# Optimization experiments

Hardware: AMD Instinct MI355X
Metric: run time of the kernel (lower is better)

The kernel has to match this reference:

```python
import jax, jax.numpy as jnp
import numpy as np

N = 50000      # num nodes
E = 800000     # num edges (before self-loops)
DIN = 256
DOUT = 256
K = 3


def setup_inputs() -> dict:
    key = jax.random.key(0)
    k1, k2, k3 = jax.random.split(key, 3)
    x = jax.random.normal(k1, (N, DIN), dtype=jnp.float32)
    edge_index = jax.random.randint(k2, (2, E), 0, N, dtype=jnp.int32)
    # xavier_uniform for weight [K+1, DIN, DOUT]
    limit = float(np.sqrt(6.0 / (DIN + DOUT)))
    weight = jax.random.uniform(k3, (K + 1, DIN, DOUT), dtype=jnp.float32,
                                minval=-limit, maxval=limit)
    bias = jnp.zeros((DOUT,), dtype=jnp.float32)
    return {"x": x, "edge_index": edge_index, "weight": weight, "bias": bias}


def reference(x, edge_index, weight, bias):
    num_nodes = x.shape[0]
    # add self loops
    loops = jnp.arange(num_nodes, dtype=edge_index.dtype)
    row = jnp.concatenate([edge_index[0], loops])
    col = jnp.concatenate([edge_index[1], loops])
    # degree of row (including self loops)
    deg = jax.ops.segment_sum(jnp.ones_like(row, dtype=x.dtype), row,
                              num_segments=num_nodes)
    deg_inv_sqrt = jnp.where(deg > 0, jax.lax.rsqrt(jnp.maximum(deg, 1e-30)), 0.0)
    # edge-weighted Laplacian values: -D^{-1/2} A D^{-1/2}, +1 on diagonal
    Lvals = -deg_inv_sqrt[row] * deg_inv_sqrt[col]
    Lvals = jnp.where(row == col, Lvals + 1.0, Lvals)

    def spmm(v):  # [N, D] -> [N, D]
        return jax.ops.segment_sum(Lvals[:, None] * v[col], row,
                                   num_segments=num_nodes)

    out = jnp.matmul(x, weight[0])
    Tx_0 = x
    Tx_1 = spmm(x)
    out = out + jnp.matmul(Tx_1, weight[1])
    for k in range(2, K + 1):
        Tx_2 = 2.0 * spmm(Tx_1) - Tx_0
        out = out + jnp.matmul(Tx_2, weight[k])
        Tx_0, Tx_1 = Tx_1, Tx_2
    return out + bias
```

## Files before the change

### kernel.cpp

```cpp
#include <hip/hip_runtime.h>
#include <hip/hip_bf16.h>

#define DFEAT 256
#define RSTRIDE 64

typedef __attribute__((ext_vector_type(8))) short bf16x8;
typedef __attribute__((ext_vector_type(4))) float f32x4;

__device__ __forceinline__ float bf2f(unsigned short u) {
  return __builtin_bit_cast(float, ((unsigned)u) << 16);
}
__device__ __forceinline__ unsigned short f2bf(float f) {
  __hip_bfloat16 h = __float2bfloat16(f);
  return *reinterpret_cast<unsigned short*>(&h);
}


__global__ void k_build(const int* __restrict__ ei0, const int* __restrict__ ei1, int E,
                        int* __restrict__ cnt, int* __restrict__ colsP) {
  int i = blockIdx.x * blockDim.x + threadIdx.x;
  if (i >= E) return;
  int r = ei0[i];
  int pos = atomicAdd(&cnt[r], 1);
  if (pos < RSTRIDE) colsP[(size_t)r * RSTRIDE + pos] = ei1[i];
}


__global__ __launch_bounds__(256) void k_f2bfwt(const float* __restrict__ x,
                                                unsigned short* __restrict__ xbf, int n4,
                                                const float* __restrict__ W,
                                                unsigned short* __restrict__ WT,
                                                const int* __restrict__ cnt,
                                                float* __restrict__ dis, int N, int nb) {
  int b = blockIdx.x;
  if (b < 256) {
    int idx = b * 256 + threadIdx.x;
    int n = idx & 255;
    int k = idx >> 8;
    float w0 = W[idx];
    float w1 = W[65536 + idx];
    float w2 = W[2 * 65536 + idx];
    float w3 = W[3 * 65536 + idx];
    int t = (n << 8) | k;
    WT[t]             = f2bf(w0 - w2);
    WT[65536 + t]     = f2bf(w1 - 3.0f * w3);
    WT[2 * 65536 + t] = f2bf(2.0f * w2);
    WT[3 * 65536 + t] = f2bf(4.0f * w3);
    return;
  }
  if (b < 256 + nb) {
    int i = (b - 256) * 256 + threadIdx.x;
    if (i < N) dis[i] = rsqrtf((float)(cnt[i] + 1));
    return;
  }
  int i = (b - 256 - nb) * 256 + threadIdx.x;
  if (i >= n4) return;
  float4 f = *(const float4*)(x + (size_t)i * 4);
  ushort4 u;
  u.x = f2bf(f.x); u.y = f2bf(f.y); u.z = f2bf(f.z); u.w = f2bf(f.w);
  *(ushort4*)(xbf + (size_t)i * 4) = u;
}


__global__ __launch_bounds__(256) void k_spmm_bf(
    const unsigned short* __restrict__ v, unsigned short* __restrict__ y,
    const int* __restrict__ cnt, const int* __restrict__ colsP,
    const float* __restrict__ dis, int N) {
  int r = blockIdx.x * 4 + (threadIdx.x >> 6);
  if (r >= N) return;
  int lane = threadIdx.x & 63;
  int fo = lane * 4;
  int len = cnt[r];
  if (len > RSTRIDE) len = RSTRIDE;
  const int* cp = colsP + (size_t)r * RSTRIDE;
  float dr = dis[r];
  float a0 = 0.f, a1 = 0.f, a2 = 0.f, a3 = 0.f;

  int e = 0;
  for (; e + 3 < len; e += 4) {
    int c0 = cp[e], c1 = cp[e + 1], c2 = cp[e + 2], c3 = cp[e + 3];
    float l0 = -dr * dis[c0] + (c0 == r ? 1.f : 0.f);
    float l1 = -dr * dis[c1] + (c1 == r ? 1.f : 0.f);
    float l2 = -dr * dis[c2] + (c2 == r ? 1.f : 0.f);
    float l3 = -dr * dis[c3] + (c3 == r ? 1.f : 0.f);
    uint2 u0 = *(const uint2*)(v + (size_t)c0 * DFEAT + fo);
    uint2 u1 = *(const uint2*)(v + (size_t)c1 * DFEAT + fo);
    uint2 u2 = *(const uint2*)(v + (size_t)c2 * DFEAT + fo);
    uint2 u3 = *(const uint2*)(v + (size_t)c3 * DFEAT + fo);
    a0 += l0 * bf2f(u0.x & 0xffff) + l1 * bf2f(u1.x & 0xffff) +
          l2 * bf2f(u2.x & 0xffff) + l3 * bf2f(u3.x & 0xffff);
    a1 += l0 * bf2f(u0.x >> 16) + l1 * bf2f(u1.x >> 16) +
          l2 * bf2f(u2.x >> 16) + l3 * bf2f(u3.x >> 16);
    a2 += l0 * bf2f(u0.y & 0xffff) + l1 * bf2f(u1.y & 0xffff) +
          l2 * bf2f(u2.y & 0xffff) + l3 * bf2f(u3.y & 0xffff);
    a3 += l0 * bf2f(u0.y >> 16) + l1 * bf2f(u1.y >> 16) +
          l2 * bf2f(u2.y >> 16) + l3 * bf2f(u3.y >> 16);
  }
  for (; e < len; ++e) {
    int c = cp[e];
    float lv = -dr * dis[c] + (c == r ? 1.f : 0.f);
    uint2 u = *(const uint2*)(v + (size_t)c * DFEAT + fo);
    a0 += lv * bf2f(u.x & 0xffff);
    a1 += lv * bf2f(u.x >> 16);
    a2 += lv * bf2f(u.y & 0xffff);
    a3 += lv * bf2f(u.y >> 16);
  }

  float sc = 1.0f - dr * dr;
  uint2 uv = *(const uint2*)(v + (size_t)r * DFEAT + fo);
  a0 += sc * bf2f(uv.x & 0xffff);
  a1 += sc * bf2f(uv.x >> 16);
  a2 += sc * bf2f(uv.y & 0xffff);
  a3 += sc * bf2f(uv.y >> 16);

  uint2 o;
  o.x = (unsigned)f2bf(a0) | ((unsigned)f2bf(a1) << 16);
  o.y = (unsigned)f2bf(a2) | ((unsigned)f2bf(a3) << 16);
  *(uint2*)(y + (size_t)r * DFEAT + fo) = o;
}


__global__ __launch_bounds__(256) void k_gemm4(
    const unsigned short* __restrict__ A0, const unsigned short* __restrict__ A1,
    const unsigned short* __restrict__ A2, const unsigned short* __restrict__ A3,
    const unsigned short* __restrict__ WT,
    const float* __restrict__ bias, float* __restrict__ C, int N) {
  int tid = threadIdx.x;
  int lane = tid & 63;
  int w = tid >> 6;
  int brow = blockIdx.x * 64;
  int arow = lane & 15;
  int kslot = (lane >> 4) * 8;

  f32x4 acc[4][4] = {};

  const unsigned short* bptr[4];
#pragma unroll
  for (int j = 0; j < 4; ++j)
    bptr[j] = WT + (size_t)(w * 64 + j * 16 + arow) * DFEAT + kslot;

#pragma unroll
  for (int g = 0; g < 4; ++g) {
    const unsigned short* Asrc = g == 0 ? A0 : g == 1 ? A1 : g == 2 ? A2 : A3;
    const unsigned short* aptr[4];
#pragma unroll
    for (int i = 0; i < 4; ++i) {
      int r = brow + i * 16 + arow;
      if (r >= N) r = N - 1;
      aptr[i] = Asrc + (size_t)r * DFEAT + kslot;
    }
    const unsigned short* bg = (const unsigned short*)((const char*)0);
#pragma unroll
    for (int ks = 0; ks < 8; ++ks) {
      bf16x8 af[4], bfr[4];
#pragma unroll
      for (int i = 0; i < 4; ++i)
        af[i] = *(const bf16x8*)(aptr[i] + ks * 32);
#pragma unroll
      for (int j = 0; j < 4; ++j)
        bfr[j] = *(const bf16x8*)(bptr[j] + (size_t)g * 65536 + ks * 32);
      __builtin_amdgcn_s_setprio(1);
#pragma unroll
      for (int i = 0; i < 4; ++i)
#pragma unroll
        for (int j = 0; j < 4; ++j)
          acc[i][j] = __builtin_amdgcn_mfma_f32_16x16x32_bf16(af[i], bfr[j], acc[i][j], 0, 0, 0);
      __builtin_amdgcn_s_setprio(0);
    }
    (void)bg;
  }

#pragma unroll
  for (int i = 0; i < 4; ++i) {
    int rowb = brow + i * 16 + (lane >> 4) * 4;
#pragma unroll
    for (int j = 0; j < 4; ++j) {
      int col = w * 64 + j * 16 + (lane & 15);
      float b = bias[col];
#pragma unroll
      for (int q = 0; q < 4; ++q) {
        int r = rowb + q;
        if (r < N) C[(size_t)r * DFEAT + col] = acc[i][j][q] + b;
      }
    }
  }
}


extern "C" void kernel_launch(void* const* d_in, const int* in_sizes, int n_in,
                              void* d_out, int out_size, void* d_ws, size_t ws_size,
                              hipStream_t stream) {
  const float* x = (const float*)d_in[0];
  const int* ei = (const int*)d_in[1];
  const float* weight = (const float*)d_in[2];
  const float* bias = (const float*)d_in[3];
  float* out = (float*)d_out;

  int N = in_sizes[0] / DFEAT;
  int E = in_sizes[1] / 2;
  const int* ei0 = ei;
  const int* ei1 = ei + E;

  char* ws = (char*)d_ws;
  size_t off = 0;
  auto alloc = [&](size_t bytes) {
    void* p = ws + off;
    off = (off + bytes + 255) & ~(size_t)255;
    return p;
  };
  int* cnt = (int*)alloc((size_t)N * sizeof(int));
  float* dis = (float*)alloc((size_t)N * sizeof(float));
  int* colsP = (int*)alloc((size_t)N * RSTRIDE * sizeof(int));
  unsigned short* xbf = (unsigned short*)alloc((size_t)N * DFEAT * 2);
  unsigned short* S1 = (unsigned short*)alloc((size_t)N * DFEAT * 2);
  unsigned short* S2 = (unsigned short*)alloc((size_t)N * DFEAT * 2);
  unsigned short* S3 = (unsigned short*)alloc((size_t)N * DFEAT * 2);
  unsigned short* WT = (unsigned short*)alloc((size_t)4 * DFEAT * DFEAT * 2);

  hipMemsetAsync(cnt, 0, (size_t)N * sizeof(int), stream);

  int eb = (E + 255) / 256;
  int nb = (N + 255) / 256;
  int n4 = N * DFEAT / 4;
  k_build<<<eb, 256, 0, stream>>>(ei0, ei1, E, cnt, colsP);
  k_f2bfwt<<<256 + nb + (n4 + 255) / 256, 256, 0, stream>>>(x, xbf, n4, weight, WT,
                                                            cnt, dis, N, nb);

  int sgrid = (N + 3) / 4;
  k_spmm_bf<<<sgrid, 256, 0, stream>>>(xbf, S1, cnt, colsP, dis, N);
  k_spmm_bf<<<sgrid, 256, 0, stream>>>(S1, S2, cnt, colsP, dis, N);
  k_spmm_bf<<<sgrid, 256, 0, stream>>>(S2, S3, cnt, colsP, dis, N);

  int ggrid = (N + 63) / 64;
  k_gemm4<<<ggrid, 256, 0, stream>>>(xbf, S1, S2, S3, WT, bias, out, N);
}
```

Baseline: 367.1 us.

## Stage GEMM A tiles through double-buffered swizzled LDS via direct global-to-LDS loads

The fused 4-term GEMM previously had each wave load A fragments straight from global memory, so all four waves fetched the same rows redundantly. A is now staged cooperatively into a double-buffered, XOR-swizzled LDS tile using global_load_lds, with the next K-chunk prefetched while MFMAs run on the current one. This removes the 4x redundant global traffic for A and overlaps loads with compute. It adds a barrier per iteration and 16 KB of LDS per block, which may reduce occupancy.

```diff
diff --git a/kernel.cpp b/kernel.cpp
--- a/kernel.cpp
+++ b/kernel.cpp
@@ -13,6 +13,11 @@
 __device__ __forceinline__ unsigned short f2bf(float f) {
   __hip_bfloat16 h = __float2bfloat16(f);
   return *reinterpret_cast<unsigned short*>(&h);
+}
+__device__ __forceinline__ void gload_lds16(const void* g, void* l) {
+  __builtin_amdgcn_global_load_lds(
+      (const __attribute__((address_space(1))) void*)g,
+      (__attribute__((address_space(3))) void*)l, 16, 0, 0);
 }
 
 
@@ -125,40 +130,56 @@
     const unsigned short* __restrict__ A2, const unsigned short* __restrict__ A3,
     const unsigned short* __restrict__ WT,
     const float* __restrict__ bias, float* __restrict__ C, int N) {
+  __shared__ __align__(16) unsigned short As[2][64 * 64];
   int tid = threadIdx.x;
   int lane = tid & 63;
   int w = tid >> 6;
   int brow = blockIdx.x * 64;
-  int arow = lane & 15;
-  int kslot = (lane >> 4) * 8;
 
   f32x4 acc[4][4] = {};
 
-  const unsigned short* bptr[4];
+  const unsigned short* bbase[4];
 #pragma unroll
   for (int j = 0; j < 4; ++j)
-    bptr[j] = WT + (size_t)(w * 64 + j * 16 + arow) * DFEAT + kslot;
-
-#pragma unroll
-  for (int g = 0; g < 4; ++g) {
+    bbase[j] = WT + (size_t)(w * 64 + j * 16 + (lane & 15)) * DFEAT + (lane >> 4) * 8;
+
+  auto stageA = [&](int buf, int it) {
+    int g = it >> 2;
+    int k0 = (it & 3) * 64;
     const unsigned short* Asrc = g == 0 ? A0 : g == 1 ? A1 : g == 2 ? A2 : A3;
-    const unsigned short* aptr[4];
-#pragma unroll
-    for (int i = 0; i < 4; ++i) {
-      int r = brow + i * 16 + arow;
-      if (r >= N) r = N - 1;
-      aptr[i] = Asrc + (size_t)r * DFEAT + kslot;
+#pragma unroll
+    for (int p = 0; p < 2; ++p) {
+      int chunk = p * 256 + w * 64 + lane;
+      int r = chunk >> 3;
+      int s = (chunk & 7) ^ (r & 7);
+      int grow = brow + r;
+      if (grow >= N) grow = N - 1;
+      gload_lds16(Asrc + (size_t)grow * DFEAT + k0 + s * 8,
+                  (char*)As[buf] + chunk * 16);
     }
-    const unsigned short* bg = (const unsigned short*)((const char*)0);
-#pragma unroll
-    for (int ks = 0; ks < 8; ++ks) {
+  };
+
+  stageA(0, 0);
+  __syncthreads();
+
+  for (int it = 0; it < 16; ++it) {
+    int cur = it & 1;
+    if (it < 15) stageA(cur ^ 1, it + 1);
+    int g = it >> 2;
+    int k0 = (it & 3) * 64;
+    size_t boff = (size_t)(g << 16) + k0;
+#pragma unroll
+    for (int ks = 0; ks < 2; ++ks) {
       bf16x8 af[4], bfr[4];
 #pragma unroll
-      for (int i = 0; i < 4; ++i)
-        af[i] = *(const bf16x8*)(aptr[i] + ks * 32);
+      for (int i = 0; i < 4; ++i) {
+        int row = i * 16 + (lane & 15);
+        int slot = (ks * 4 + (lane >> 4)) ^ (row & 7);
+        af[i] = *(const bf16x8*)((const char*)As[cur] + row * 128 + slot * 16);
+      }
 #pragma unroll
       for (int j = 0; j < 4; ++j)
-        bfr[j] = *(const bf16x8*)(bptr[j] + (size_t)g * 65536 + ks * 32);
+        bfr[j] = *(const bf16x8*)(bbase[j] + boff + ks * 32);
       __builtin_amdgcn_s_setprio(1);
 #pragma unroll
       for (int i = 0; i < 4; ++i)
@@ -167,7 +188,7 @@
           acc[i][j] = __builtin_amdgcn_mfma_f32_16x16x32_bf16(af[i], bfr[j], acc[i][j], 0, 0, 0);
       __builtin_amdgcn_s_setprio(0);
     }
-    (void)bg;
+    if (it < 15) __syncthreads();
   }
 
 #pragma unroll
```

Measured after the change: 331.8 us. -9.6%, faster.
